# Kernel tuning notes

Hardware: AMD Instinct MI355X
Metric: run time of the kernel (lower is better)

Reference implementation:

```python
import jax, jax.numpy as jnp
import numpy as np

D_MODEL = 1024
N_HEAD = 16
D_QKV = 64
B, L = 2, 2048
LN_EPS = 1e-5


def setup_inputs() -> dict:
    key = jax.random.key(0)
    ks = jax.random.split(key, 5)
    # xavier-normal-ish scale for [H, d_model, d_qkv] params
    std_in = (2.0 / (D_MODEL + D_QKV)) ** 0.5
    return {
        "x": jax.random.normal(ks[0], (B, L, D_MODEL), jnp.float32),
        "w_q": jax.random.normal(ks[1], (N_HEAD, D_MODEL, D_QKV), jnp.float32) * std_in,
        "w_k": jax.random.normal(ks[2], (N_HEAD, D_MODEL, D_QKV), jnp.float32) * std_in,
        "w_v": jax.random.normal(ks[3], (N_HEAD, D_MODEL, D_QKV), jnp.float32) * std_in,
        "w_o": jax.random.normal(ks[4], (N_HEAD, D_QKV, D_MODEL), jnp.float32) * std_in,
        "ln_gamma": jnp.ones((D_MODEL,), jnp.float32),
        "ln_beta": jnp.zeros((D_MODEL,), jnp.float32),
    }


def reference(x, w_q, w_k, w_v, w_o, ln_gamma, ln_beta):
    # q,k,v: [B, H, L, d_qkv]
    q = jnp.einsum('hmq,blm->bhlq', w_q, x)
    k = jnp.einsum('hmq,blm->bhlq', w_k, x)
    v = jnp.einsum('hmq,blm->bhlq', w_v, x)
    # scores: [B, H, L, L]
    s = jnp.einsum('bhiq,bhjq->bhij', q, k) / (D_QKV ** 0.5)
    s = jax.nn.softmax(s, axis=-1)
    # (dropout disabled: eval-mode reference)
    att = jnp.einsum('bhij,bhjq->bhiq', s, v)          # [B, H, L, d_qkv]
    out = jnp.einsum('bhlq,hqm->blm', att, w_o)        # [B, L, d_model]
    y = x + out                                        # residual
    mu = jnp.mean(y, axis=-1, keepdims=True)
    var = jnp.var(y, axis=-1, keepdims=True)
    return (y - mu) * jax.lax.rsqrt(var + LN_EPS) * ln_gamma + ln_beta
```

## Files before the change

### kernel.cpp

```cpp
#include <hip/hip_runtime.h>
#include <hip/hip_bf16.h>
#include <cstdint>

#define B_      2
#define L_      2048
#define DM_     1024
#define H_      16
#define DQ_     64
#define LN_EPS  1e-5f
#define QSCALE  0.1803368801111204f

typedef unsigned short u16;
typedef unsigned int   u32;
typedef __attribute__((ext_vector_type(8)))  short short8;
typedef __attribute__((ext_vector_type(4)))  unsigned short u16x4;
typedef __attribute__((ext_vector_type(4)))  unsigned int   u32x4;
typedef __attribute__((ext_vector_type(4)))  float f32x4;
typedef __attribute__((ext_vector_type(16))) float f32x16;

__device__ __forceinline__ u16 f2b(float f) {
  __hip_bfloat16 h = __float2bfloat16(f);
  return *reinterpret_cast<u16*>(&h);
}
__device__ __forceinline__ u32 pk2(float lo, float hi) {
  return (u32)f2b(lo) | ((u32)f2b(hi) << 16);
}

__device__ __forceinline__ void gl_lds16(const void* g, void* l) {
  auto gp = reinterpret_cast<const __attribute__((address_space(1))) unsigned int*>(
      reinterpret_cast<uintptr_t>(g));
  auto lp = reinterpret_cast<__attribute__((address_space(3))) unsigned int*>(
      reinterpret_cast<uintptr_t>(l));
  __builtin_amdgcn_global_load_lds(gp, lp, 16, 0, 0);
}

__device__ __forceinline__ short8 frag8(const u16* base, int row, int lchunk) {
  return *(const short8*)(base + row * 64 + ((lchunk ^ (row & 7)) << 3));
}

__global__ __launch_bounds__(256) void prep_all(
    const float* __restrict__ x, const float* __restrict__ wq,
    const float* __restrict__ wk, const float* __restrict__ wv,
    const float* __restrict__ wo, u16* __restrict__ xb,
    u16* __restrict__ wt, u16* __restrict__ wot) {
  __shared__ float Ls[64][65];
  const int t = threadIdx.x;
  const int bx = blockIdx.x;
  if (bx < 4096) {
    int i = bx * 256 + t;
    float4 v = ((const float4*)x)[i];
    u16x4 o = { f2b(v.x), f2b(v.y), f2b(v.z), f2b(v.w) };
    *(u16x4*)(xb + (size_t)i * 4) = o;
  } else if (bx < 4096 + 768) {
    int b2 = bx - 4096;
    int mt = b2 & 15, h = (b2 >> 4) & 15, wh = b2 >> 8;
    const float* in = ((wh == 0) ? wq : (wh == 1) ? wk : wv) + (size_t)h * DM_ * DQ_;
    #pragma unroll
    for (int i = 0; i < 16; ++i) {
      int idx = i * 256 + t, r = idx >> 6, c = idx & 63;
      Ls[r][c] = in[(size_t)(mt * 64 + r) * DQ_ + c];
    }
    __syncthreads();
    u16* outb = wt + (size_t)(wh * H_ + h) * DQ_ * DM_;
    #pragma unroll
    for (int i = 0; i < 16; ++i) {
      int idx = i * 256 + t, q = idx >> 6, mm = idx & 63;
      outb[(size_t)q * DM_ + mt * 64 + mm] = f2b(Ls[mm][q]);
    }
  } else {
    int b3 = bx - 4864;
    int mt = b3 & 15, kt = b3 >> 4;
    #pragma unroll
    for (int i = 0; i < 16; ++i) {
      int idx = i * 256 + t, r = idx >> 6, c = idx & 63;
      Ls[r][c] = wo[(size_t)(kt * 64 + r) * DM_ + mt * 64 + c];
    }
    __syncthreads();
    #pragma unroll
    for (int i = 0; i < 16; ++i) {
      int idx = i * 256 + t, mm = idx >> 6, kk = idx & 63;
      wot[(size_t)(mt * 64 + mm) * DM_ + kt * 64 + kk] = f2b(Ls[kk][mm]);
    }
  }
}

__global__ __launch_bounds__(256) void qkv_big(const u16* __restrict__ xb,
    const u16* __restrict__ wt, u16* __restrict__ Q, u16* __restrict__ K,
    u16* __restrict__ Vtg) {
  const int nt = blockIdx.x, mt = blockIdx.y;
  __shared__ __align__(16) u16 SH[128 * 136];
  u16* As_ = SH;
  u16* Bs_ = SH + 8192;
  const int t = threadIdx.x, w = t >> 6, lane = t & 63;
  const int lx = lane & 15, lq = lane >> 4;
  const int row0 = mt * 128, n0 = nt * 128;
  const int r8 = lane >> 3, lc = (lane & 7) ^ r8;

  const u16* gA = xb + (size_t)(row0 + w * 32 + r8) * DM_ + lc * 8;
  const u16* gB = wt + (size_t)(n0  + w * 32 + r8) * DM_ + lc * 8;
  u16* lA = As_ + (w * 32) * 64;
  u16* lB = Bs_ + (w * 32) * 64;

  f32x4 z = {0.f, 0.f, 0.f, 0.f};
  f32x4 acc[2][8];
  #pragma unroll
  for (int mb = 0; mb < 2; ++mb)
    #pragma unroll
    for (int nb = 0; nb < 8; ++nb) acc[mb][nb] = z;

  for (int k0 = 0; k0 < DM_; k0 += 64) {
    #pragma unroll
    for (int i = 0; i < 4; ++i) {
      gl_lds16(gA + (size_t)i * 8 * DM_ + k0, lA + i * 8 * 64);
      gl_lds16(gB + (size_t)i * 8 * DM_ + k0, lB + i * 8 * 64);
    }
    __syncthreads();
    short8 af[2][2];
    #pragma unroll
    for (int mb = 0; mb < 2; ++mb)
      #pragma unroll
      for (int kh = 0; kh < 2; ++kh)
        af[mb][kh] = frag8(As_, w * 32 + mb * 16 + lx, (kh << 2) | lq);
    #pragma unroll
    for (int nb = 0; nb < 8; ++nb) {
      short8 b0 = frag8(Bs_, nb * 16 + lx, lq);
      short8 b1 = frag8(Bs_, nb * 16 + lx, 4 | lq);
      acc[0][nb] = __builtin_amdgcn_mfma_f32_16x16x32_bf16(af[0][0], b0, acc[0][nb], 0, 0, 0);
      acc[0][nb] = __builtin_amdgcn_mfma_f32_16x16x32_bf16(af[0][1], b1, acc[0][nb], 0, 0, 0);
      acc[1][nb] = __builtin_amdgcn_mfma_f32_16x16x32_bf16(af[1][0], b0, acc[1][nb], 0, 0, 0);
      acc[1][nb] = __builtin_amdgcn_mfma_f32_16x16x32_bf16(af[1][1], b1, acc[1][nb], 0, 0, 0);
    }
    __syncthreads();
  }

  const int wh = n0 >> 10;
  const float oscale = (wh == 0) ? QSCALE : 1.0f;
  const int bb = row0 >> 11, l0 = row0 & 2047;
  const int hd0 = n0 & 1023;
  u16* Ep = SH;

  if (wh != 2) {
    #pragma unroll
    for (int mb = 0; mb < 2; ++mb)
      #pragma unroll
      for (int nb = 0; nb < 8; ++nb)
        #pragma unroll
        for (int r = 0; r < 4; ++r) {
          int l = w * 32 + mb * 16 + lq * 4 + r;
          Ep[l * 136 + nb * 16 + lx] = f2b(acc[mb][nb][r] * oscale);
        }
    __syncthreads();
    u16* outp = (wh == 0) ? Q : K;
    #pragma unroll
    for (int hs = 0; hs < 2; ++hs) {
      const int hh = (hd0 >> 6) + hs;
      u16* gbase = outp + ((size_t)(bb * H_ + hh) * L_ + l0) * DQ_;
      #pragma unroll
      for (int it = 0; it < 4; ++it) {
        int u = it * 256 + t;
        int l = u >> 3, chunk = u & 7;
        *(uint4*)(gbase + u * 8) = *(const uint4*)&Ep[l * 136 + hs * 64 + chunk * 8];
      }
    }
  } else {
    #pragma unroll
    for (int mb = 0; mb < 2; ++mb)
      #pragma unroll
      for (int nb = 0; nb < 8; ++nb) {
        int l = w * 32 + mb * 16 + lq * 4;
        int lp = (l & ~12) | ((l & 4) << 1) | ((l & 8) >> 1);
        uint2 pv = { pk2(acc[mb][nb][0], acc[mb][nb][1]),
                     pk2(acc[mb][nb][2], acc[mb][nb][3]) };
        *(uint2*)&Ep[(nb * 16 + lx) * 136 + lp] = pv;
      }
    __syncthreads();
    #pragma unroll
    for (int it = 0; it < 8; ++it) {
      int v = it * 256 + t;
      int dloc = v >> 4, chunk = v & 15;
      int hh = (hd0 + dloc) >> 6, dd = (hd0 + dloc) & 63;
      u16* g = Vtg + ((size_t)(bb * H_ + hh) * DQ_ + dd) * L_ + l0 + chunk * 8;
      *(uint4*)g = *(const uint4*)&Ep[dloc * 136 + chunk * 8];
    }
  }
}

__global__ __launch_bounds__(512) void attn_mfma(const u16* __restrict__ Q,
    const u16* __restrict__ K, const u16* __restrict__ Vtg, u16* __restrict__ att) {
  const int qt = blockIdx.x, h = blockIdx.y, b = blockIdx.z;
  __shared__ __align__(16) u16 Qs_[256 * 64];
  __shared__ __align__(16) u16 Ks_[2][64 * 64];
  __shared__ __align__(16) u16 Vt_[2][64 * 64];
  const int t = threadIdx.x, w = t >> 6, lane = t & 63;
  const int c = lane & 31, lsel = lane >> 5;
  const int r8 = lane >> 3, lc = (lane & 7) ^ r8;
  const size_t bh  = (size_t)(b * H_ + h) * L_ * DQ_;
  const size_t bhv = (size_t)(b * H_ + h) * DQ_ * L_;

  const u16* gQ = Q + bh + (size_t)(qt * 256 + w * 32 + r8) * DQ_ + lc * 8;
  #pragma unroll
  for (int i = 0; i < 4; ++i) gl_lds16(gQ + (size_t)i * 8 * DQ_, Qs_ + (w * 32 + i * 8) * 64);

  const u16* gK = K   + bh  + (size_t)(w * 8 + r8) * DQ_ + lc * 8;
  const u16* gV = Vtg + bhv + (size_t)(w * 8 + r8) * L_  + lc * 8;

  gl_lds16(gK, Ks_[0] + w * 8 * 64);
  gl_lds16(gV, Vt_[0] + w * 8 * 64);
  __syncthreads();
  short8 qb[4];
  #pragma unroll
  for (int km = 0; km < 4; ++km) qb[km] = frag8(Qs_, w * 32 + c, (km << 1) | lsel);

  f32x16 zz = {0.f,0.f,0.f,0.f,0.f,0.f,0.f,0.f,0.f,0.f,0.f,0.f,0.f,0.f,0.f,0.f};
  f32x16 oacc0 = zz, oacc1 = zz, lacc = zz;
  const short one_bf = (short)0x3F80;
  short8 ones = {one_bf, one_bf, one_bf, one_bf, one_bf, one_bf, one_bf, one_bf};

  for (int kt = 0; kt < L_ / 64; ++kt) {
    const int cur = kt & 1;
    __syncthreads();

    if (kt + 1 < L_ / 64) {
      const int nxt = 1 - cur;
      gl_lds16(gK + (size_t)(kt + 1) * 64 * DQ_, Ks_[nxt] + w * 8 * 64);
      gl_lds16(gV + (size_t)(kt + 1) * 64,       Vt_[nxt] + w * 8 * 64);
    }

    u32x4 paw[4];
    #pragma unroll
    for (int kb = 0; kb < 2; ++kb) {
      f32x16 s = zz;
      #pragma unroll
      for (int km = 0; km < 4; ++km) {
        short8 ka = frag8(Ks_[cur], kb * 32 + c, (km << 1) | lsel);
        s = __builtin_amdgcn_mfma_f32_32x32x16_bf16(ka, qb[km], s, 0, 0, 0);
      }
      #pragma unroll
      for (int F = 0; F < 2; ++F) {
        u32x4 pw;
        #pragma unroll
        for (int i = 0; i < 4; ++i) {
          float p0 = __builtin_amdgcn_exp2f(s[8 * F + 2 * i]);
          float p1 = __builtin_amdgcn_exp2f(s[8 * F + 2 * i + 1]);
          pw[i] = __builtin_amdgcn_perm(__float_as_uint(p1), __float_as_uint(p0), 0x07060302u);
        }
        paw[2 * kb + F] = pw;
      }
    }

    #pragma unroll
    for (int km = 0; km < 4; ++km) {
      short8 pa  = *reinterpret_cast<const short8*>(&paw[km]);
      short8 vb0 = frag8(Vt_[cur], c,      (km << 1) | lsel);
      short8 vb1 = frag8(Vt_[cur], 32 + c, (km << 1) | lsel);
      oacc0 = __builtin_amdgcn_mfma_f32_32x32x16_bf16(pa, vb0, oacc0, 0, 0, 0);
      oacc1 = __builtin_amdgcn_mfma_f32_32x32x16_bf16(pa, vb1, oacc1, 0, 0, 0);
      lacc  = __builtin_amdgcn_mfma_f32_32x32x16_bf16(pa, ones, lacc, 0, 0, 0);
    }
  }

  const int qrow_base = qt * 256 + w * 32;
  #pragma unroll
  for (int r = 0; r < 16; ++r) {
    int qr = (r & 3) + 8 * (r >> 2) + 4 * lsel;
    float inv = 1.0f / lacc[r];
    size_t base = (size_t)(b * L_ + qrow_base + qr) * DM_ + h * DQ_;
    att[base + c]      = f2b(oacc0[r] * inv);
    att[base + 32 + c] = f2b(oacc1[r] * inv);
  }
}

__global__ __launch_bounds__(256) void oproj_big(const u16* __restrict__ A,
    const u16* __restrict__ wot, float* __restrict__ out) {
  const int nt = blockIdx.x, mt = blockIdx.y;
  __shared__ __align__(16) u16 As_[128 * 64];
  __shared__ __align__(16) u16 Bs_[64 * 64];
  const int t = threadIdx.x, w = t >> 6, lane = t & 63;
  const int lx = lane & 15, lq = lane >> 4;
  const int row0 = mt * 128, n0 = nt * 64;
  const int r8 = lane >> 3, lc = (lane & 7) ^ r8;

  const u16* gA = A   + (size_t)(row0 + w * 32 + r8) * DM_ + lc * 8;
  const u16* gB = wot + (size_t)(n0  + w * 16 + r8) * DM_ + lc * 8;
  u16* lA = As_ + (w * 32) * 64;
  u16* lB = Bs_ + (w * 16) * 64;

  f32x4 z = {0.f, 0.f, 0.f, 0.f};
  f32x4 acc[2][4];
  #pragma unroll
  for (int mb = 0; mb < 2; ++mb)
    #pragma unroll
    for (int nb = 0; nb < 4; ++nb) acc[mb][nb] = z;

  for (int k0 = 0; k0 < DM_; k0 += 64) {
    #pragma unroll
    for (int i = 0; i < 4; ++i)
      gl_lds16(gA + (size_t)i * 8 * DM_ + k0, lA + i * 8 * 64);
    #pragma unroll
    for (int i = 0; i < 2; ++i)
      gl_lds16(gB + (size_t)i * 8 * DM_ + k0, lB + i * 8 * 64);
    __syncthreads();
    short8 af[2][2];
    #pragma unroll
    for (int mb = 0; mb < 2; ++mb)
      #pragma unroll
      for (int kh = 0; kh < 2; ++kh)
        af[mb][kh] = frag8(As_, w * 32 + mb * 16 + lx, (kh << 2) | lq);
    #pragma unroll
    for (int nb = 0; nb < 4; ++nb) {
      short8 b0 = frag8(Bs_, nb * 16 + lx, lq);
      short8 b1 = frag8(Bs_, nb * 16 + lx, 4 | lq);
      acc[0][nb] = __builtin_amdgcn_mfma_f32_16x16x32_bf16(af[0][0], b0, acc[0][nb], 0, 0, 0);
      acc[0][nb] = __builtin_amdgcn_mfma_f32_16x16x32_bf16(af[0][1], b1, acc[0][nb], 0, 0, 0);
      acc[1][nb] = __builtin_amdgcn_mfma_f32_16x16x32_bf16(af[1][0], b0, acc[1][nb], 0, 0, 0);
      acc[1][nb] = __builtin_amdgcn_mfma_f32_16x16x32_bf16(af[1][1], b1, acc[1][nb], 0, 0, 0);
    }
    __syncthreads();
  }
  #pragma unroll
  for (int mb = 0; mb < 2; ++mb)
    #pragma unroll
    for (int nb = 0; nb < 4; ++nb)
      #pragma unroll
      for (int r = 0; r < 4; ++r) {
        int row = row0 + w * 32 + mb * 16 + lq * 4 + r;
        out[(size_t)row * DM_ + n0 + nb * 16 + lx] = acc[mb][nb][r];
      }
}

__global__ __launch_bounds__(256) void resid_ln(
    const float* __restrict__ x, const float* __restrict__ gamma,
    const float* __restrict__ beta, float* __restrict__ out) {
  const int row = blockIdx.x;
  const int t   = threadIdx.x;
  const float4* xp = (const float4*)(x   + (size_t)row * DM_);
  float4*       yp = (float4*)      (out + (size_t)row * DM_);

  float4 xv = xp[t];
  float4 av = yp[t];
  float y0 = xv.x + av.x, y1 = xv.y + av.y, y2 = xv.z + av.z, y3 = xv.w + av.w;

  float s  = y0 + y1 + y2 + y3;
  float s2 = y0 * y0 + y1 * y1 + y2 * y2 + y3 * y3;
  #pragma unroll
  for (int off = 32; off > 0; off >>= 1) {
    s  += __shfl_xor(s,  off, 64);
    s2 += __shfl_xor(s2, off, 64);
  }
  __shared__ float red[8];
  const int wave = t >> 6, lane = t & 63;
  if (lane == 0) { red[wave] = s; red[4 + wave] = s2; }
  __syncthreads();
  s  = red[0] + red[1] + red[2] + red[3];
  s2 = red[4] + red[5] + red[6] + red[7];

  const float mean = s * (1.f / DM_);
  const float var  = s2 * (1.f / DM_) - mean * mean;
  const float inv  = rsqrtf(var + LN_EPS);

  const float4 g  = ((const float4*)gamma)[t];
  const float4 bt = ((const float4*)beta)[t];
  float4 r;
  r.x = (y0 - mean) * inv * g.x + bt.x;
  r.y = (y1 - mean) * inv * g.y + bt.y;
  r.z = (y2 - mean) * inv * g.z + bt.z;
  r.w = (y3 - mean) * inv * g.w + bt.w;
  yp[t] = r;
}

extern "C" void kernel_launch(void* const* d_in, const int* in_sizes, int n_in,
                              void* d_out, int out_size, void* d_ws, size_t ws_size,
                              hipStream_t stream) {
  const float* x     = (const float*)d_in[0];
  const float* wq    = (const float*)d_in[1];
  const float* wk    = (const float*)d_in[2];
  const float* wv    = (const float*)d_in[3];
  const float* wo    = (const float*)d_in[4];
  const float* gamma = (const float*)d_in[5];
  const float* beta  = (const float*)d_in[6];
  float* out = (float*)d_out;

  char* ws = (char*)d_ws;
  u16* xb  = (u16*)ws;
  u16* Qb  = (u16*)(ws + ((size_t)8  << 20));
  u16* Kb  = (u16*)(ws + ((size_t)16 << 20));
  u16* Vtg = (u16*)(ws + ((size_t)24 << 20));
  u16* wt  = (u16*)(ws + ((size_t)32 << 20));
  u16* wot = (u16*)(ws + ((size_t)38 << 20));
  u16* att = (u16*)(ws + ((size_t)40 << 20));

  prep_all <<<5120, 256, 0, stream>>>(x, wq, wk, wv, wo, xb, wt, wot);
  qkv_big  <<<dim3(24, 32),    256, 0, stream>>>(xb, wt, Qb, Kb, Vtg);
  attn_mfma<<<dim3(L_ / 256, H_, B_), 512, 0, stream>>>(Qb, Kb, Vtg, att);
  oproj_big<<<dim3(16, 32),    256, 0, stream>>>(att, wot, out);
  resid_ln <<<B_ * L_, 256, 0, stream>>>(x, gamma, beta, out);
}
```

Baseline: 187.6 us.

## Enlarge QKV GEMM tile to 256x128 with 32x32 MFMA and direct stores

```diff
diff --git a/kernel.cpp b/kernel.cpp
--- a/kernel.cpp
+++ b/kernel.cpp
@@ -88,101 +88,64 @@
     const u16* __restrict__ wt, u16* __restrict__ Q, u16* __restrict__ K,
     u16* __restrict__ Vtg) {
   const int nt = blockIdx.x, mt = blockIdx.y;
-  __shared__ __align__(16) u16 SH[128 * 136];
-  u16* As_ = SH;
-  u16* Bs_ = SH + 8192;
+  __shared__ __align__(16) u16 As_[256 * 64];
+  __shared__ __align__(16) u16 Bs_[128 * 64];
   const int t = threadIdx.x, w = t >> 6, lane = t & 63;
-  const int lx = lane & 15, lq = lane >> 4;
-  const int row0 = mt * 128, n0 = nt * 128;
+  const int c = lane & 31, lsel = lane >> 5;
   const int r8 = lane >> 3, lc = (lane & 7) ^ r8;
-
-  const u16* gA = xb + (size_t)(row0 + w * 32 + r8) * DM_ + lc * 8;
+  const int row0 = mt * 256, n0 = nt * 128;
+
+  const u16* gA = xb + (size_t)(row0 + w * 64 + r8) * DM_ + lc * 8;
   const u16* gB = wt + (size_t)(n0  + w * 32 + r8) * DM_ + lc * 8;
-  u16* lA = As_ + (w * 32) * 64;
+  u16* lA = As_ + (w * 64) * 64;
   u16* lB = Bs_ + (w * 32) * 64;
 
-  f32x4 z = {0.f, 0.f, 0.f, 0.f};
-  f32x4 acc[2][8];
-  #pragma unroll
-  for (int mb = 0; mb < 2; ++mb)
-    #pragma unroll
-    for (int nb = 0; nb < 8; ++nb) acc[mb][nb] = z;
+  f32x16 zz = {0.f,0.f,0.f,0.f,0.f,0.f,0.f,0.f,0.f,0.f,0.f,0.f,0.f,0.f,0.f,0.f};
+  f32x16 acc[2][4] = {{zz, zz, zz, zz}, {zz, zz, zz, zz}};
 
   for (int k0 = 0; k0 < DM_; k0 += 64) {
     #pragma unroll
-    for (int i = 0; i < 4; ++i) {
+    for (int i = 0; i < 8; ++i)
       gl_lds16(gA + (size_t)i * 8 * DM_ + k0, lA + i * 8 * 64);
+    #pragma unroll
+    for (int i = 0; i < 4; ++i)
       gl_lds16(gB + (size_t)i * 8 * DM_ + k0, lB + i * 8 * 64);
-    }
-    __syncthreads();
-    short8 af[2][2];
-    #pragma unroll
-    for (int mb = 0; mb < 2; ++mb)
-      #pragma unroll
-      for (int kh = 0; kh < 2; ++kh)
-        af[mb][kh] = frag8(As_, w * 32 + mb * 16 + lx, (kh << 2) | lq);
-    #pragma unroll
-    for (int nb = 0; nb < 8; ++nb) {
-      short8 b0 = frag8(Bs_, nb * 16 + lx, lq);
-      short8 b1 = frag8(Bs_, nb * 16 + lx, 4 | lq);
-      acc[0][nb] = __builtin_amdgcn_mfma_f32_16x16x32_bf16(af[0][0], b0, acc[0][nb], 0, 0, 0);
-      acc[0][nb] = __builtin_amdgcn_mfma_f32_16x16x32_bf16(af[0][1], b1, acc[0][nb], 0, 0, 0);
-      acc[1][nb] = __builtin_amdgcn_mfma_f32_16x16x32_bf16(af[1][0], b0, acc[1][nb], 0, 0, 0);
-      acc[1][nb] = __builtin_amdgcn_mfma_f32_16x16x32_bf16(af[1][1], b1, acc[1][nb], 0, 0, 0);
-    }
-    __syncthreads();
-  }
-
-  const int wh = n0 >> 10;
+    __syncthreads();
+    #pragma unroll
+    for (int km = 0; km < 4; ++km) {
+      short8 a0 = frag8(As_, w * 64 + c,      (km << 1) | lsel);
+      short8 a1 = frag8(As_, w * 64 + 32 + c, (km << 1) | lsel);
+      #pragma unroll
+      for (int ct = 0; ct < 4; ++ct) {
+        short8 b = frag8(Bs_, ct * 32 + c, (km << 1) | lsel);
+        acc[0][ct] = __builtin_amdgcn_mfma_f32_32x32x16_bf16(a0, b, acc[0][ct], 0, 0, 0);
+        acc[1][ct] = __builtin_amdgcn_mfma_f32_32x32x16_bf16(a1, b, acc[1][ct], 0, 0, 0);
+      }
+    }
+    __syncthreads();
+  }
+
+  const int wh = nt >> 3;
   const float oscale = (wh == 0) ? QSCALE : 1.0f;
-  const int bb = row0 >> 11, l0 = row0 & 2047;
-  const int hd0 = n0 & 1023;
-  u16* Ep = SH;
-
-  if (wh != 2) {
-    #pragma unroll
-    for (int mb = 0; mb < 2; ++mb)
-      #pragma unroll
-      for (int nb = 0; nb < 8; ++nb)
-        #pragma unroll
-        for (int r = 0; r < 4; ++r) {
-          int l = w * 32 + mb * 16 + lq * 4 + r;
-          Ep[l * 136 + nb * 16 + lx] = f2b(acc[mb][nb][r] * oscale);
+  u16* qk = (wh == 0) ? Q : K;
+  #pragma unroll
+  for (int rb = 0; rb < 2; ++rb)
+    #pragma unroll
+    for (int ct = 0; ct < 4; ++ct)
+      #pragma unroll
+      for (int r = 0; r < 16; ++r) {
+        int m_row = row0 + w * 64 + rb * 32 + (r & 3) + 8 * (r >> 2) + 4 * lsel;
+        int bb = m_row >> 11, l = m_row & 2047;
+        int n = (n0 & 1023) + ct * 32 + c;
+        int hh = n >> 6, d = n & 63;
+        u16 val = f2b(acc[rb][ct][r] * oscale);
+        if (wh == 2) {
+          int lp = (l & ~12) | ((l & 4) << 1) | ((l & 8) >> 1);
+          Vtg[((size_t)(bb * H_ + hh) * DQ_ + d) * L_ + lp] = val;
+        } else {
+          qk[((size_t)(bb * H_ + hh) * L_ + l) * DQ_ + d] = val;
         }
-    __syncthreads();
-    u16* outp = (wh == 0) ? Q : K;
-    #pragma unroll
-    for (int hs = 0; hs < 2; ++hs) {
-      const int hh = (hd0 >> 6) + hs;
-      u16* gbase = outp + ((size_t)(bb * H_ + hh) * L_ + l0) * DQ_;
-      #pragma unroll
-      for (int it = 0; it < 4; ++it) {
-        int u = it * 256 + t;
-        int l = u >> 3, chunk = u & 7;
-        *(uint4*)(gbase + u * 8) = *(const uint4*)&Ep[l * 136 + hs * 64 + chunk * 8];
-      }
-    }
-  } else {
-    #pragma unroll
-    for (int mb = 0; mb < 2; ++mb)
-      #pragma unroll
-      for (int nb = 0; nb < 8; ++nb) {
-        int l = w * 32 + mb * 16 + lq * 4;
-        int lp = (l & ~12) | ((l & 4) << 1) | ((l & 8) >> 1);
-        uint2 pv = { pk2(acc[mb][nb][0], acc[mb][nb][1]),
-                     pk2(acc[mb][nb][2], acc[mb][nb][3]) };
-        *(uint2*)&Ep[(nb * 16 + lx) * 136 + lp] = pv;
-      }
-    __syncthreads();
-    #pragma unroll
-    for (int it = 0; it < 8; ++it) {
-      int v = it * 256 + t;
-      int dloc = v >> 4, chunk = v & 15;
-      int hh = (hd0 + dloc) >> 6, dd = (hd0 + dloc) & 63;
-      u16* g = Vtg + ((size_t)(bb * H_ + hh) * DQ_ + dd) * L_ + l0 + chunk * 8;
-      *(uint4*)g = *(const uint4*)&Ep[dloc * 136 + chunk * 8];
-    }
-  }
+      }
 }
 
 __global__ __launch_bounds__(512) void attn_mfma(const u16* __restrict__ Q,
@@ -390,7 +353,7 @@
   u16* att = (u16*)(ws + ((size_t)40 << 20));
 
   prep_all <<<5120, 256, 0, stream>>>(x, wq, wk, wv, wo, xb, wt, wot);
-  qkv_big  <<<dim3(24, 32),    256, 0, stream>>>(xb, wt, Qb, Kb, Vtg);
+  qkv_big  <<<dim3(24, 16),    256, 0, stream>>>(xb, wt, Qb, Kb, Vtg);
   attn_mfma<<<dim3(L_ / 256, H_, B_), 512, 0, stream>>>(Qb, Kb, Vtg, att);
   oproj_big<<<dim3(16, 32),    256, 0, stream>>>(att, wot, out);
   resid_ln <<<B_ * L_, 256, 0, stream>>>(x, gamma, beta, out);
```

New measurement: 219.0 us. +16.8%, slower.
